# Kernel tuning notes

Measured on AMD Instinct MI355X. Metric: run time of the kernel, lower is better.

The kernel has to match this reference:

```python
import jax, jax.numpy as jnp
import numpy as np

BS, N, J, F = 8, 1024, 4, 32
N_CLASSES = 2


def setup_inputs() -> dict:
    key = jax.random.key(0)
    k1, k2, k3, k4 = jax.random.split(key, 4)
    WW = jax.random.normal(k1, (BS, N, N, J), dtype=jnp.float32)
    x = jax.random.normal(k2, (BS, N, F), dtype=jnp.float32)
    # nn.Linear(J*F, n_classes): weight (n_classes, J*F), bias (n_classes,)
    bound = 1.0 / np.sqrt(J * F)
    fc_w = jax.random.uniform(k3, (N_CLASSES, J * F), minval=-bound, maxval=bound, dtype=jnp.float32)
    fc_b = jax.random.uniform(k4, (N_CLASSES,), minval=-bound, maxval=bound, dtype=jnp.float32)
    return {"WW": WW, "x": x, "fc_w": fc_w, "fc_b": fc_b}


def reference(WW, x, fc_w, fc_b):
    bs, n, _, j = WW.shape
    f = x.shape[-1]
    # GMul: out[b,n,j*F+f] = sum_m W[b,n,m,j] * x[b,m,f]
    h = jnp.einsum('bnmj,bmf->bnjf', WW, x).reshape(bs, n, j * f)
    # Linear over last dim
    out = h @ fc_w.T + fc_b  # (bs, N, n_classes)
    return out
```

## Files before the change

kernel.cpp:

```cpp
#include <hip/hip_runtime.h>

#define BS 8
#define NN 1024
#define JJ 4
#define FF 32
#define NC 2

__global__ void __launch_bounds__(256) compute_y_kernel(
    const float* __restrict__ x, const float* __restrict__ fc_w,
    float* __restrict__ y) {
    int idx = blockIdx.x * blockDim.x + threadIdx.x;
    if (idx >= BS * NN * JJ) return;
    int j  = idx & (JJ - 1);
    int bm = idx >> 2;
    const float* xr = x + (size_t)bm * FF;
    const float* w0 = fc_w + 0 * (JJ * FF) + j * FF;
    const float* w1 = fc_w + 1 * (JJ * FF) + j * FF;
    float a0 = 0.f, a1 = 0.f;
#pragma unroll
    for (int f = 0; f < FF; ++f) {
        float xv = xr[f];
        a0 += xv * w0[f];
        a1 += xv * w1[f];
    }
    reinterpret_cast<float2*>(y)[idx] = make_float2(a0, a1);
}

__global__ void __launch_bounds__(256) reduce_out_kernel(
    const float* __restrict__ WW, const float* __restrict__ y,
    const float* __restrict__ fc_b, float* __restrict__ out) {
    const int wave = threadIdx.x >> 6;
    const int lane = threadIdx.x & 63;
    const int gid  = blockIdx.x * 4 + wave;
    const int b    = gid >> 10;

    const float4* W4 = reinterpret_cast<const float4*>(WW + (size_t)gid * (NN * JJ));
    const float4* Y4 = reinterpret_cast<const float4*>(y + (size_t)b * (NN * JJ * NC));

    float a0 = 0.f, a1 = 0.f;
#pragma unroll 4
    for (int m = lane; m < NN; m += 64) {
        float4 w  = W4[m];
        float4 y0 = Y4[m * 2];
        float4 y1 = Y4[m * 2 + 1];
        a0 += w.x * y0.x + w.y * y0.z + w.z * y1.x + w.w * y1.z;
        a1 += w.x * y0.y + w.y * y0.w + w.z * y1.y + w.w * y1.w;
    }
#pragma unroll
    for (int off = 32; off > 0; off >>= 1) {
        a0 += __shfl_down(a0, off, 64);
        a1 += __shfl_down(a1, off, 64);
    }
    if (lane == 0) {
        out[(size_t)gid * NC + 0] = a0 + fc_b[0];
        out[(size_t)gid * NC + 1] = a1 + fc_b[1];
    }
}

extern "C" void kernel_launch(void* const* d_in, const int* in_sizes, int n_in,
                              void* d_out, int out_size, void* d_ws, size_t ws_size,
                              hipStream_t stream) {
    const float* WW   = (const float*)d_in[0];
    const float* x    = (const float*)d_in[1];
    const float* fc_w = (const float*)d_in[2];
    const float* fc_b = (const float*)d_in[3];
    float* out = (float*)d_out;
    float* y   = (float*)d_ws;

    {
        int total = BS * NN * JJ;
        compute_y_kernel<<<(total + 255) / 256, 256, 0, stream>>>(x, fc_w, y);
    }
    {
        int blocks = (BS * NN) / 4;
        reduce_out_kernel<<<blocks, 256, 0, stream>>>(WW, y, fc_b, out);
    }
}
```

Before: 30.90 us.

## Stage y in LDS, process two rows per wave, use nontemporal WW loads

The reduce kernel now copies the per-batch projected y vectors into shared memory, split into two planar float4 arrays. Each wave then handles two output rows, so every y value fetched from LDS feeds twice as many FMAs. WW, which is streamed once, is read with nontemporal loads so it does not evict reusable data from cache. The price is 32KB of LDS per block, which can cap occupancy, plus a block-wide sync before the streaming loop, in a kernel that is mostly limited by the 128MB WW read.

Result: no change. 30.59 us (-1.0%).

```diff
diff --git a/kernel.cpp b/kernel.cpp
--- a/kernel.cpp
+++ b/kernel.cpp
@@ -6,9 +6,11 @@
 #define FF 32
 #define NC 2
 
+typedef float f4v __attribute__((ext_vector_type(4)));
+
 __global__ void __launch_bounds__(256) compute_y_kernel(
     const float* __restrict__ x, const float* __restrict__ fc_w,
-    float* __restrict__ y) {
+    float2* __restrict__ yA, float2* __restrict__ yB) {
     int idx = blockIdx.x * blockDim.x + threadIdx.x;
     if (idx >= BS * NN * JJ) return;
     int j  = idx & (JJ - 1);
@@ -23,37 +25,58 @@
         a0 += xv * w0[f];
         a1 += xv * w1[f];
     }
-    reinterpret_cast<float2*>(y)[idx] = make_float2(a0, a1);
+    float2 v = make_float2(a0, a1);
+    if (j < 2) yA[bm * 2 + j]       = v;
+    else       yB[bm * 2 + (j - 2)] = v;
 }
 
 __global__ void __launch_bounds__(256) reduce_out_kernel(
-    const float* __restrict__ WW, const float* __restrict__ y,
-    const float* __restrict__ fc_b, float* __restrict__ out) {
+    const float* __restrict__ WW, const float4* __restrict__ yA,
+    const float4* __restrict__ yB, const float* __restrict__ fc_b,
+    float* __restrict__ out) {
+    __shared__ float4 lyA[NN];
+    __shared__ float4 lyB[NN];
+
+    const int blk  = blockIdx.x;
+    const int b    = blk >> 7;
     const int wave = threadIdx.x >> 6;
     const int lane = threadIdx.x & 63;
-    const int gid  = blockIdx.x * 4 + wave;
-    const int b    = gid >> 10;
 
-    const float4* W4 = reinterpret_cast<const float4*>(WW + (size_t)gid * (NN * JJ));
-    const float4* Y4 = reinterpret_cast<const float4*>(y + (size_t)b * (NN * JJ * NC));
+    for (int i = threadIdx.x; i < NN; i += 256) {
+        lyA[i] = yA[(size_t)b * NN + i];
+        lyB[i] = yB[(size_t)b * NN + i];
+    }
+    __syncthreads();
 
-    float a0 = 0.f, a1 = 0.f;
+    const int row0 = blk * 8 + wave * 2;
+    const f4v* W0 = reinterpret_cast<const f4v*>(WW) + (size_t)row0 * NN;
+    const f4v* W1 = W0 + NN;
+
+    float a00 = 0.f, a01 = 0.f, a10 = 0.f, a11 = 0.f;
 #pragma unroll 4
     for (int m = lane; m < NN; m += 64) {
-        float4 w  = W4[m];
-        float4 y0 = Y4[m * 2];
-        float4 y1 = Y4[m * 2 + 1];
-        a0 += w.x * y0.x + w.y * y0.z + w.z * y1.x + w.w * y1.z;
-        a1 += w.x * y0.y + w.y * y0.w + w.z * y1.y + w.w * y1.w;
+        f4v w0 = __builtin_nontemporal_load(W0 + m);
+        f4v w1 = __builtin_nontemporal_load(W1 + m);
+        float4 ya = lyA[m];
+        float4 yb = lyB[m];
+        a00 += w0.x * ya.x + w0.y * ya.z + w0.z * yb.x + w0.w * yb.z;
+        a01 += w0.x * ya.y + w0.y * ya.w + w0.z * yb.y + w0.w * yb.w;
+        a10 += w1.x * ya.x + w1.y * ya.z + w1.z * yb.x + w1.w * yb.z;
+        a11 += w1.x * ya.y + w1.y * ya.w + w1.z * yb.y + w1.w * yb.w;
     }
 #pragma unroll
     for (int off = 32; off > 0; off >>= 1) {
-        a0 += __shfl_down(a0, off, 64);
-        a1 += __shfl_down(a1, off, 64);
+        a00 += __shfl_down(a00, off, 64);
+        a01 += __shfl_down(a01, off, 64);
+        a10 += __shfl_down(a10, off, 64);
+        a11 += __shfl_down(a11, off, 64);
     }
     if (lane == 0) {
-        out[(size_t)gid * NC + 0] = a0 + fc_b[0];
-        out[(size_t)gid * NC + 1] = a1 + fc_b[1];
+        float b0 = fc_b[0], b1 = fc_b[1];
+        out[(size_t)row0 * NC + 0] = a00 + b0;
+        out[(size_t)row0 * NC + 1] = a01 + b1;
+        out[(size_t)(row0 + 1) * NC + 0] = a10 + b0;
+        out[(size_t)(row0 + 1) * NC + 1] = a11 + b1;
     }
 }
 
@@ -65,14 +88,18 @@
     const float* fc_w = (const float*)d_in[2];
     const float* fc_b = (const float*)d_in[3];
     float* out = (float*)d_out;
-    float* y   = (float*)d_ws;
+
+    float* ws  = (float*)d_ws;
+    float2* yA2 = (float2*)ws;
+    float2* yB2 = (float2*)(ws + (size_t)BS * NN * 4);
 
     {
         int total = BS * NN * JJ;
-        compute_y_kernel<<<(total + 255) / 256, 256, 0, stream>>>(x, fc_w, y);
+        compute_y_kernel<<<(total + 255) / 256, 256, 0, stream>>>(x, fc_w, yA2, yB2);
     }
     {
-        int blocks = (BS * NN) / 4;
-        reduce_out_kernel<<<blocks, 256, 0, stream>>>(WW, y, fc_b, out);
+        int blocks = (BS * NN) / 8;
+        reduce_out_kernel<<<blocks, 256, 0, stream>>>(
+            WW, (const float4*)yA2, (const float4*)yB2, fc_b, out);
     }
 }
```
